# Optimization experiments

Hardware: AMD Instinct MI355X
Metric: run time of the kernel (lower is better)

Reference implementation:

```python
import jax, jax.numpy as jnp
import numpy as np


def setup_inputs() -> dict:
    key = jax.random.key(0)
    k1, k2, k3, k4, k5 = jax.random.split(key, 5)
    B, S, I, O, R = 4, 2048, 4096, 4096, 16
    s = 1.0 / np.sqrt(I)
    return {
        "x": jax.random.normal(k1, (B, S, I), dtype=jnp.float32),
        "W": jax.random.normal(k2, (O, I), dtype=jnp.float32) * s,
        "b": jax.random.normal(k3, (O,), dtype=jnp.float32) * 0.02,
        "lora_A": jax.random.normal(k4, (I, R), dtype=jnp.float32) * s,
        "lora_B": jax.random.normal(k5, (R, O), dtype=jnp.float32) * 0.02,
    }


def reference(x, W, b, lora_A, lora_B):
    # Base linear: F.linear(x, W, b) = x @ W.T + b   -> [B, S, O]
    base_out = jnp.einsum("bsi,oi->bso", x, W) + b
    # LoRA low-rank delta: (x @ A) @ B  -> [B, S, O]
    lora_out = jnp.einsum("bsr,ro->bso", jnp.einsum("bsi,ir->bsr", x, lora_A), lora_B)
    return base_out + lora_out
```

## Files before the change

### kernel.cpp

```cpp
#include <hip/hip_runtime.h>

typedef float f32x4 __attribute__((ext_vector_type(4)));
typedef __bf16 bf16x8 __attribute__((ext_vector_type(8)));
typedef __bf16 bf16x4 __attribute__((ext_vector_type(4)));

#define GLOBAL_AS __attribute__((address_space(1)))
#define LDS_AS    __attribute__((address_space(3)))

static __device__ __forceinline__ void gload16(const void* g, void* l) {
  __builtin_amdgcn_global_load_lds((const GLOBAL_AS void*)g, (LDS_AS void*)l, 16, 0, 0);
}

#define BAR() __builtin_amdgcn_s_barrier()
#define WAITL0() do { asm volatile("s_waitcnt lgkmcnt(0)" ::: "memory"); __builtin_amdgcn_sched_barrier(0); } while (0)

__global__ __launch_bounds__(256)
void xa_cvt(const float* __restrict__ X, const float* __restrict__ A,
            __bf16* __restrict__ Xb, __bf16* __restrict__ XAb) {
  constexpr int K = 4096, TM = 16, KC = 64;
  __shared__ float Xs[TM][68];
  __shared__ float Asm[KC][16];
  const int t = threadIdx.x;
  const int m0 = blockIdx.x * TM;
  const int crow = t >> 4, rr = t & 15;
  float acc = 0.f;
  for (int k0 = 0; k0 < K; k0 += KC) {
    f32x4 v = *reinterpret_cast<const f32x4*>(X + (size_t)(m0 + crow) * K + k0 + rr * 4);
    *reinterpret_cast<f32x4*>(&Xs[crow][rr * 4]) = v;
    bf16x4 p;
#pragma unroll
    for (int e = 0; e < 4; ++e) p[e] = (__bf16)v[e];
    *reinterpret_cast<bf16x4*>(Xb + (size_t)(m0 + crow) * K + k0 + rr * 4) = p;
    {
      int row = t >> 2, c4 = (t & 3) * 4;
      *reinterpret_cast<f32x4*>(&Asm[row][c4]) =
          *reinterpret_cast<const f32x4*>(A + (size_t)(k0 + row) * 16 + c4);
    }
    __syncthreads();
#pragma unroll 16
    for (int kk = 0; kk < KC; ++kk) acc += Xs[crow][kk] * Asm[kk][rr];
    __syncthreads();
  }
  const size_t base = (size_t)(m0 + crow) * 64;
  XAb[base + rr] = (__bf16)acc;
  XAb[base + 16 + rr] = (__bf16)0.f;
  XAb[base + 32 + rr] = (__bf16)0.f;
  XAb[base + 48 + rr] = (__bf16)0.f;
}

__global__ __launch_bounds__(256)
void cvt_f32_bf16(const float* __restrict__ in, __bf16* __restrict__ out, long n4) {
  long i = (long)blockIdx.x * blockDim.x + threadIdx.x;
  long stride = (long)gridDim.x * blockDim.x;
  for (; i < n4; i += stride) {
    f32x4 v = reinterpret_cast<const f32x4*>(in)[i];
    bf16x4 p;
#pragma unroll
    for (int e = 0; e < 4; ++e) p[e] = (__bf16)v[e];
    reinterpret_cast<bf16x4*>(out)[i] = p;
  }
}

__global__ __launch_bounds__(256)
void blt64(const float* __restrict__ Bl, __bf16* __restrict__ BlT) {
  int idx = blockIdx.x * 256 + threadIdx.x;
  int col = idx >> 6, k = idx & 63;
  float v = (k < 16) ? Bl[(size_t)k * 4096 + col] : 0.f;
  BlT[idx] = (__bf16)v;
}

__global__ __launch_bounds__(512, 2)
void gemm8(const __bf16* __restrict__ Xb, const __bf16* __restrict__ Wb,
           const __bf16* __restrict__ XAb, const __bf16* __restrict__ BlT,
           const float* __restrict__ bias, float* __restrict__ out) {
  constexpr int N = 4096, K = 4096;
  __shared__ __align__(16) char sm[131072];
  char* Asm_ = sm;
  char* Bsm_ = sm + 65536;

  const int t = threadIdx.x;
  const int lane = t & 63, w = t >> 6;
  const int wr = w >> 2, wc = w & 3;
  const int fr = lane & 15, fg = lane >> 4;

  const int bid = blockIdx.x;
  const int xcd = bid & 7, l = bid >> 3;
  const int mt = (xcd << 2) | ((l >> 4) & 2) | (l & 1);
  const int nt = (l >> 1) & 15;
  const int m0 = mt * 256, n0 = nt * 256;

  const int sRow = w * 16 + (lane >> 2);
  const int sColB = (((lane & 3) ^ ((lane >> 3) & 3)) << 4);
  const int rdOff = fr * 64 + ((fg ^ ((fr >> 1) & 3)) << 4);
  const int rdOffA = wr * 16384 + rdOff;
  const int rdOffB = (wc >> 1) * 16384 + (wc & 1) * 8192 + rdOff;

  auto stageA = [&](int h, int tt) {
    char* dst = Asm_ + (tt & 1) * 32768 + h * 16384 + w * 2048;
    const char* g;
    if (tt < 64) g = (const char*)(Xb + (size_t)(m0 + h * 128 + sRow) * K + (size_t)tt * 64) + sColB;
    else         g = (const char*)(XAb + (size_t)(m0 + h * 128 + sRow) * 64) + sColB;
    gload16(g, dst);
    gload16(g + 64, dst + 1024);
  };
  auto stageB = [&](int h, int tt) {
    char* dst = Bsm_ + (tt & 1) * 32768 + h * 16384 + w * 2048;
    const char* g;
    if (tt < 64) g = (const char*)(Wb + (size_t)(n0 + h * 128 + sRow) * K + (size_t)tt * 64) + sColB;
    else         g = (const char*)(BlT + (size_t)(n0 + h * 128 + sRow) * 64) + sColB;
    gload16(g, dst);
    gload16(g + 64, dst + 1024);
  };

  auto rdA = [&](int b, int mf, int kk) -> bf16x8 {
    return *reinterpret_cast<const bf16x8*>(Asm_ + b * 32768 + (mf * 2 + kk) * 1024 + rdOffA);
  };
  auto rdB = [&](int b, int nf, int kk) -> bf16x8 {
    return *reinterpret_cast<const bf16x8*>(Bsm_ + b * 32768 + (nf * 2 + kk) * 1024 + rdOffB);
  };

  f32x4 acc[8][4];
#pragma unroll
  for (int i = 0; i < 8; ++i)
#pragma unroll
    for (int j = 0; j < 4; ++j) acc[i][j] = (f32x4)0.f;

  bf16x8 aF[4][2], bL[2][2], bH[2][2];

  auto MF = [&](bf16x8 (&af)[4][2], bf16x8 (&bf_)[2][2], int mi, int ni) {
#pragma unroll
    for (int i = 0; i < 4; ++i)
#pragma unroll
      for (int j = 0; j < 2; ++j)
#pragma unroll
        for (int kk = 0; kk < 2; ++kk)
          acc[mi * 4 + i][ni * 2 + j] = __builtin_amdgcn_mfma_f32_16x16x32_bf16(
              af[i][kk], bf_[j][kk], acc[mi * 4 + i][ni * 2 + j], 0, 0, 0);
  };

  auto tile_step = [&](int tv) {
    const int b = tv & 1;
#pragma unroll
    for (int i = 0; i < 4; ++i)
#pragma unroll
      for (int kk = 0; kk < 2; ++kk) aF[i][kk] = rdA(b, i, kk);
#pragma unroll
    for (int j = 0; j < 2; ++j)
#pragma unroll
      for (int kk = 0; kk < 2; ++kk) bL[j][kk] = rdB(b, j, kk);
    stageA(0, tv + 1);
    BAR(); WAITL0();
    __builtin_amdgcn_s_setprio(1); MF(aF, bL, 0, 0); __builtin_amdgcn_s_setprio(0);
    BAR();
#pragma unroll
    for (int j = 0; j < 2; ++j)
#pragma unroll
      for (int kk = 0; kk < 2; ++kk) bH[j][kk] = rdB(b, 2 + j, kk);
    stageA(1, tv + 1);
    BAR(); WAITL0();
    __builtin_amdgcn_s_setprio(1); MF(aF, bH, 0, 1); __builtin_amdgcn_s_setprio(0);
    BAR();
#pragma unroll
    for (int i = 0; i < 4; ++i)
#pragma unroll
      for (int kk = 0; kk < 2; ++kk) aF[i][kk] = rdA(b, 4 + i, kk);
    if (tv + 2 <= 64) stageB(0, tv + 2);
    BAR(); WAITL0();
    __builtin_amdgcn_s_setprio(1); MF(aF, bH, 1, 1); __builtin_amdgcn_s_setprio(0);
    BAR();
    if (tv + 2 <= 64) stageB(1, tv + 2);
    BAR(); WAITL0();
    __builtin_amdgcn_s_setprio(1); MF(aF, bL, 1, 0); __builtin_amdgcn_s_setprio(0);
    asm volatile("s_waitcnt vmcnt(4)" ::: "memory");
    BAR();
  };

  stageA(0, 0); stageA(1, 0); stageB(0, 0); stageB(1, 0); stageB(0, 1); stageB(1, 1);
  asm volatile("s_waitcnt vmcnt(4)" ::: "memory");
  BAR();

  for (int tp = 0; tp < 32; ++tp) { tile_step(2 * tp); tile_step(2 * tp + 1); }

  asm volatile("s_waitcnt vmcnt(0)" ::: "memory");
  BAR();
  {
#pragma unroll
    for (int i = 0; i < 4; ++i)
#pragma unroll
      for (int kk = 0; kk < 2; ++kk) aF[i][kk] = rdA(0, i, kk);
#pragma unroll
    for (int j = 0; j < 2; ++j)
#pragma unroll
      for (int kk = 0; kk < 2; ++kk) { bL[j][kk] = rdB(0, j, kk); bH[j][kk] = rdB(0, 2 + j, kk); }
    MF(aF, bL, 0, 0); MF(aF, bH, 0, 1);
#pragma unroll
    for (int i = 0; i < 4; ++i)
#pragma unroll
      for (int kk = 0; kk < 2; ++kk) aF[i][kk] = rdA(0, 4 + i, kk);
    MF(aF, bH, 1, 1); MF(aF, bL, 1, 0);
  }

  float bb[4];
#pragma unroll
  for (int j = 0; j < 4; ++j) bb[j] = bias[n0 + wc * 64 + j * 16 + fr];
#pragma unroll
  for (int i = 0; i < 8; ++i) {
    const int row0 = m0 + wr * 128 + i * 16 + fg * 4;
#pragma unroll
    for (int j = 0; j < 4; ++j) {
      const int col = n0 + wc * 64 + j * 16 + fr;
#pragma unroll
      for (int q = 0; q < 4; ++q)
        out[(size_t)(row0 + q) * N + col] = acc[i][j][q] + bb[j];
    }
  }
}

extern "C" void kernel_launch(void* const* d_in, const int* in_sizes, int n_in,
                              void* d_out, int out_size, void* d_ws, size_t ws_size,
                              hipStream_t stream) {
  const float* x  = (const float*)d_in[0];
  const float* W  = (const float*)d_in[1];
  const float* b  = (const float*)d_in[2];
  const float* lA = (const float*)d_in[3];
  const float* lB = (const float*)d_in[4];
  float* out = (float*)d_out;

  char* ws = (char*)d_ws;
  __bf16* Xb  = (__bf16*)ws;
  __bf16* Wb  = (__bf16*)(ws + 67108864);
  __bf16* XAb = (__bf16*)(ws + 100663296);
  __bf16* BlT = (__bf16*)(ws + 101711872);

  xa_cvt<<<8192 / 16, 256, 0, stream>>>(x, lA, Xb, XAb);
  cvt_f32_bf16<<<1024, 256, 0, stream>>>(W, Wb, (long)4096 * 4096 / 4);
  blt64<<<4096 * 64 / 256, 256, 0, stream>>>(lB, BlT);

  gemm8<<<dim3(512), dim3(512), 0, stream>>>(Xb, Wb, XAb, BlT, b, out);
}
```

Baseline: 338.5 us.

## Prefetch A tiles earlier in GEMM pipeline and vectorize preprocessing kernels

The GEMM main loop now issues the next tile's A-half-1 load at the start of each step and the A-half-0 load for two tiles ahead at the end. This deepens the prefetch distance for A, and the vmcnt waits are adjusted to match. The final tile is peeled out of the loop. The xa_cvt kernel now computes the X·A product using transposed LDS storage and f32x4 dot-product accumulation, and the W conversion kernel handles 8 elements per thread. The deeper pipeline keeps more loads in flight, and the reordered LDS buffer reuse carries a risk of hazards if the waits or barriers are off.

Measured after the change: 336.4 us. No clear change (-0.6%).

```diff
diff --git a/kernel.cpp b/kernel.cpp
--- a/kernel.cpp
+++ b/kernel.cpp
@@ -19,45 +19,50 @@
             __bf16* __restrict__ Xb, __bf16* __restrict__ XAb) {
   constexpr int K = 4096, TM = 16, KC = 64;
   __shared__ float Xs[TM][68];
-  __shared__ float Asm[KC][16];
+  __shared__ float At[16][68];
   const int t = threadIdx.x;
   const int m0 = blockIdx.x * TM;
-  const int crow = t >> 4, rr = t & 15;
-  float acc = 0.f;
+  const int lrow = t >> 4, c4 = (t & 15) * 4;
+  const int orow = t >> 4, oc = t & 15;
+  const int akk = t >> 2, ar4 = (t & 3) * 4;
+  f32x4 av = (f32x4)0.f;
   for (int k0 = 0; k0 < K; k0 += KC) {
-    f32x4 v = *reinterpret_cast<const f32x4*>(X + (size_t)(m0 + crow) * K + k0 + rr * 4);
-    *reinterpret_cast<f32x4*>(&Xs[crow][rr * 4]) = v;
+    const float* gx = X + (size_t)(m0 + lrow) * K + k0 + c4;
+    f32x4 u = *reinterpret_cast<const f32x4*>(gx);
+    *reinterpret_cast<f32x4*>(&Xs[lrow][c4]) = u;
     bf16x4 p;
 #pragma unroll
-    for (int e = 0; e < 4; ++e) p[e] = (__bf16)v[e];
-    *reinterpret_cast<bf16x4*>(Xb + (size_t)(m0 + crow) * K + k0 + rr * 4) = p;
-    {
-      int row = t >> 2, c4 = (t & 3) * 4;
-      *reinterpret_cast<f32x4*>(&Asm[row][c4]) =
-          *reinterpret_cast<const f32x4*>(A + (size_t)(k0 + row) * 16 + c4);
+    for (int e = 0; e < 4; ++e) p[e] = (__bf16)u[e];
+    *reinterpret_cast<bf16x4*>(Xb + (size_t)(m0 + lrow) * K + k0 + c4) = p;
+    f32x4 a = *reinterpret_cast<const f32x4*>(A + (size_t)(k0 + akk) * 16 + ar4);
+    At[ar4 + 0][akk] = a[0]; At[ar4 + 1][akk] = a[1];
+    At[ar4 + 2][akk] = a[2]; At[ar4 + 3][akk] = a[3];
+    __syncthreads();
+#pragma unroll
+    for (int q = 0; q < 16; ++q) {
+      f32x4 xv = *reinterpret_cast<const f32x4*>(&Xs[orow][q * 4]);
+      av += xv * *reinterpret_cast<const f32x4*>(&At[oc][q * 4]);
     }
     __syncthreads();
-#pragma unroll 16
-    for (int kk = 0; kk < KC; ++kk) acc += Xs[crow][kk] * Asm[kk][rr];
-    __syncthreads();
-  }
-  const size_t base = (size_t)(m0 + crow) * 64;
-  XAb[base + rr] = (__bf16)acc;
-  XAb[base + 16 + rr] = (__bf16)0.f;
-  XAb[base + 32 + rr] = (__bf16)0.f;
-  XAb[base + 48 + rr] = (__bf16)0.f;
+  }
+  const float acc = av[0] + av[1] + av[2] + av[3];
+  const size_t base = (size_t)(m0 + orow) * 64;
+  XAb[base + oc] = (__bf16)acc;
+#pragma unroll
+  for (int z = 0; z < 3; ++z) XAb[base + 16 + z * 16 + oc] = (__bf16)0.f;
 }
 
 __global__ __launch_bounds__(256)
-void cvt_f32_bf16(const float* __restrict__ in, __bf16* __restrict__ out, long n4) {
+void cvt_f32_bf16(const float* __restrict__ in, __bf16* __restrict__ out, long n8) {
   long i = (long)blockIdx.x * blockDim.x + threadIdx.x;
   long stride = (long)gridDim.x * blockDim.x;
-  for (; i < n4; i += stride) {
-    f32x4 v = reinterpret_cast<const f32x4*>(in)[i];
-    bf16x4 p;
-#pragma unroll
-    for (int e = 0; e < 4; ++e) p[e] = (__bf16)v[e];
-    reinterpret_cast<bf16x4*>(out)[i] = p;
+  for (; i < n8; i += stride) {
+    f32x4 u = reinterpret_cast<const f32x4*>(in)[2 * i];
+    f32x4 v = reinterpret_cast<const f32x4*>(in)[2 * i + 1];
+    bf16x8 p;
+#pragma unroll
+    for (int e = 0; e < 4; ++e) { p[e] = (__bf16)u[e]; p[4 + e] = (__bf16)v[e]; }
+    reinterpret_cast<bf16x8*>(out)[i] = p;
   }
 }
 
@@ -148,7 +153,7 @@
     for (int j = 0; j < 2; ++j)
 #pragma unroll
       for (int kk = 0; kk < 2; ++kk) bL[j][kk] = rdB(b, j, kk);
-    stageA(0, tv + 1);
+    stageA(1, tv + 1);
     BAR(); WAITL0();
     __builtin_amdgcn_s_setprio(1); MF(aF, bL, 0, 0); __builtin_amdgcn_s_setprio(0);
     BAR();
@@ -156,7 +161,6 @@
     for (int j = 0; j < 2; ++j)
 #pragma unroll
       for (int kk = 0; kk < 2; ++kk) bH[j][kk] = rdB(b, 2 + j, kk);
-    stageA(1, tv + 1);
     BAR(); WAITL0();
     __builtin_amdgcn_s_setprio(1); MF(aF, bH, 0, 1); __builtin_amdgcn_s_setprio(0);
     BAR();
@@ -164,25 +168,58 @@
     for (int i = 0; i < 4; ++i)
 #pragma unroll
       for (int kk = 0; kk < 2; ++kk) aF[i][kk] = rdA(b, 4 + i, kk);
-    if (tv + 2 <= 64) stageB(0, tv + 2);
+    stageB(0, tv + 2);
     BAR(); WAITL0();
     __builtin_amdgcn_s_setprio(1); MF(aF, bH, 1, 1); __builtin_amdgcn_s_setprio(0);
     BAR();
-    if (tv + 2 <= 64) stageB(1, tv + 2);
+    stageB(1, tv + 2);
+    stageA(0, tv + 2);
     BAR(); WAITL0();
     __builtin_amdgcn_s_setprio(1); MF(aF, bL, 1, 0); __builtin_amdgcn_s_setprio(0);
-    asm volatile("s_waitcnt vmcnt(4)" ::: "memory");
-    BAR();
-  };
-
-  stageA(0, 0); stageA(1, 0); stageB(0, 0); stageB(1, 0); stageB(0, 1); stageB(1, 1);
-  asm volatile("s_waitcnt vmcnt(4)" ::: "memory");
+    asm volatile("s_waitcnt vmcnt(6)" ::: "memory");
+    BAR();
+  };
+
+  stageA(0, 0); stageA(1, 0); stageB(0, 0); stageB(1, 0);
+  stageB(0, 1); stageB(1, 1); stageA(0, 1);
+  asm volatile("s_waitcnt vmcnt(6)" ::: "memory");
   BAR();
 
-  for (int tp = 0; tp < 32; ++tp) { tile_step(2 * tp); tile_step(2 * tp + 1); }
-
-  asm volatile("s_waitcnt vmcnt(0)" ::: "memory");
-  BAR();
+  for (int tv = 0; tv < 63; ++tv) tile_step(tv);
+
+  {
+    const int b = 1;
+#pragma unroll
+    for (int i = 0; i < 4; ++i)
+#pragma unroll
+      for (int kk = 0; kk < 2; ++kk) aF[i][kk] = rdA(b, i, kk);
+#pragma unroll
+    for (int j = 0; j < 2; ++j)
+#pragma unroll
+      for (int kk = 0; kk < 2; ++kk) bL[j][kk] = rdB(b, j, kk);
+    stageA(1, 64);
+    BAR(); WAITL0();
+    __builtin_amdgcn_s_setprio(1); MF(aF, bL, 0, 0); __builtin_amdgcn_s_setprio(0);
+    BAR();
+#pragma unroll
+    for (int j = 0; j < 2; ++j)
+#pragma unroll
+      for (int kk = 0; kk < 2; ++kk) bH[j][kk] = rdB(b, 2 + j, kk);
+    BAR(); WAITL0();
+    __builtin_amdgcn_s_setprio(1); MF(aF, bH, 0, 1); __builtin_amdgcn_s_setprio(0);
+    BAR();
+#pragma unroll
+    for (int i = 0; i < 4; ++i)
+#pragma unroll
+      for (int kk = 0; kk < 2; ++kk) aF[i][kk] = rdA(b, 4 + i, kk);
+    BAR(); WAITL0();
+    __builtin_amdgcn_s_setprio(1); MF(aF, bH, 1, 1); __builtin_amdgcn_s_setprio(0);
+    BAR();
+    __builtin_amdgcn_s_setprio(1); MF(aF, bL, 1, 0); __builtin_amdgcn_s_setprio(0);
+    asm volatile("s_waitcnt vmcnt(0)" ::: "memory");
+    BAR();
+  }
+
   {
 #pragma unroll
     for (int i = 0; i < 4; ++i)
@@ -233,7 +270,7 @@
   __bf16* BlT = (__bf16*)(ws + 101711872);
 
   xa_cvt<<<8192 / 16, 256, 0, stream>>>(x, lA, Xb, XAb);
-  cvt_f32_bf16<<<1024, 256, 0, stream>>>(W, Wb, (long)4096 * 4096 / 4);
+  cvt_f32_bf16<<<1024, 256, 0, stream>>>(W, Wb, (long)4096 * 4096 / 8);
   blt64<<<4096 * 64 / 256, 256, 0, stream>>>(lB, BlT);
 
   gemm8<<<dim3(512), dim3(512), 0, stream>>>(Xb, Wb, XAb, BlT, b, out);
```
